# Kernel optimization log

Measured on AMD Instinct MI355X. Metric: run time of the kernel, lower is better.

Reference implementation:

```python
import jax, jax.numpy as jnp
import numpy as np

D_MODEL = 2048
HEADS = 16


def setup_inputs() -> dict:
    key = jax.random.key(0)
    ks = jax.random.split(key, 9)
    s = 1.0 / np.sqrt(D_MODEL)
    x = jax.random.normal(ks[0], (2, 2048, D_MODEL), dtype=jnp.float32)
    wq = jax.random.uniform(ks[1], (D_MODEL, D_MODEL), jnp.float32, -s, s)
    wk = jax.random.uniform(ks[2], (D_MODEL, D_MODEL), jnp.float32, -s, s)
    wv = jax.random.uniform(ks[3], (D_MODEL, D_MODEL), jnp.float32, -s, s)
    wo = jax.random.uniform(ks[4], (D_MODEL, D_MODEL), jnp.float32, -s, s)
    bq = jax.random.uniform(ks[5], (D_MODEL,), jnp.float32, -s, s)
    bk = jax.random.uniform(ks[6], (D_MODEL,), jnp.float32, -s, s)
    bv = jax.random.uniform(ks[7], (D_MODEL,), jnp.float32, -s, s)
    bo = jax.random.uniform(ks[8], (D_MODEL,), jnp.float32, -s, s)
    return {"x": x, "wq": wq, "bq": bq, "wk": wk, "bk": bk,
            "wv": wv, "bv": bv, "wo": wo, "bo": bo}


def _split(t, heads):
    b, s, d = t.shape
    return t.reshape(b, s, heads, d // heads).transpose(0, 2, 1, 3)  # [b,h,s,dh]


def reference(x, wq, bq, wk, bk, wv, bv, wo, bo):
    q = x @ wq.T + bq
    k = x @ wk.T + bk
    v = x @ wv.T + bv
    q, k, v = _split(q, HEADS), _split(k, HEADS), _split(v, HEADS)
    dh = q.shape[-1]
    scale = 1.0 / np.sqrt(dh).astype(np.float32)
    score = jnp.einsum('bhqd,bhkd->bhqk', q, k) * scale  # [b,h,s,s]
    score = jax.nn.softmax(score.astype(jnp.float32), axis=-1).astype(q.dtype)
    out = jnp.einsum('bhqk,bhkd->bhqd', score, v)
    b, h, s, _ = out.shape
    out = out.transpose(0, 2, 1, 3).reshape(b, s, h * dh)
    return out @ wo.T + bo
```

## Files before the change

kernel.cpp:

```cpp
#include <hip/hip_runtime.h>
#include <cstdint>
#include <cstddef>

#define D_MODEL 2048
#define SEQ 2048
#define BATCH 2
#define HEADS 16
#define DH 128
#define MROWS (BATCH * SEQ)

typedef __attribute__((ext_vector_type(8))) short short8;
typedef __attribute__((ext_vector_type(4))) float f32x4;
typedef __attribute__((ext_vector_type(16))) float f32x16;
typedef __attribute__((ext_vector_type(2))) unsigned int uint2e;

__device__ __forceinline__ unsigned short f2bf(float f) {
    unsigned int u = __builtin_bit_cast(unsigned int, f);
    u += 0x7fffu + ((u >> 16) & 1u);
    return (unsigned short)(u >> 16);
}

__device__ __forceinline__ unsigned int cvt_pk_bf16(float lo, float hi) {
    unsigned int w;
    asm("v_cvt_pk_bf16_f32 %0, %1, %2" : "=v"(w) : "v"(lo), "v"(hi));
    return w;
}

__device__ __forceinline__ void swap32(unsigned int& x, unsigned int& y) {
#if __has_builtin(__builtin_amdgcn_permlane32_swap)
    uint2e r = __builtin_amdgcn_permlane32_swap(x, y, false, false);
    x = r[0]; y = r[1];
#else
    const int hi = (threadIdx.x >> 5) & 1;
    const unsigned int gx = (unsigned int)__shfl_xor((int)x, 32);
    const unsigned int gy = (unsigned int)__shfl_xor((int)y, 32);
    const unsigned int nx = hi ? gy : x;
    const unsigned int ny = hi ? y : gx;
    x = nx; y = ny;
#endif
}

__device__ __forceinline__ void gload_lds16(const unsigned short* g, unsigned short* l) {
    __builtin_amdgcn_global_load_lds(
        (const __attribute__((address_space(1))) void*)g,
        (__attribute__((address_space(3))) void*)l, 16, 0, 0);
}

__global__ __launch_bounds__(256) void cvt_kernel(const float* __restrict__ in,
                                                  unsigned short* __restrict__ out, int n4) {
    int i = blockIdx.x * 256 + threadIdx.x;
    if (i < n4) {
        const float4 v = reinterpret_cast<const float4*>(in)[i];
        ushort4 o;
        o.x = f2bf(v.x); o.y = f2bf(v.y); o.z = f2bf(v.z); o.w = f2bf(v.w);
        reinterpret_cast<ushort4*>(out)[i] = o;
    }
}

__global__ __launch_bounds__(256) void cvt4_kernel(const float* __restrict__ w0,
                                                   const float* __restrict__ w1,
                                                   const float* __restrict__ w2,
                                                   const float* __restrict__ w3,
                                                   unsigned short* __restrict__ out) {
    const int per = (D_MODEL * D_MODEL) / 4;
    int i = blockIdx.x * 256 + threadIdx.x;
    const int sel = i / per;
    const int off = i - sel * per;
    const float* s = sel == 0 ? w0 : sel == 1 ? w1 : sel == 2 ? w2 : w3;
    const float4 v = reinterpret_cast<const float4*>(s)[off];
    ushort4 o;
    o.x = f2bf(v.x); o.y = f2bf(v.y); o.z = f2bf(v.z); o.w = f2bf(v.w);
    reinterpret_cast<ushort4*>(out)[i] = o;
}

__global__ __launch_bounds__(512, 2)
void gemm8qk(const unsigned short* __restrict__ A,
             const unsigned short* __restrict__ W0,
             const unsigned short* __restrict__ W1,
             const float* __restrict__ b0f,
             const float* __restrict__ b1f,
             unsigned short* __restrict__ O0,
             unsigned short* __restrict__ O1) {
    constexpr int BK = 64;
    constexpr int K = D_MODEL;
    constexpr int NT_N = 16;
    constexpr int NWG = 16 * NT_N;
    __shared__ unsigned short As[2][16384];
    __shared__ unsigned short Bs[2][16384];

    const int tid  = threadIdx.x;
    const int lane = tid & 63;
    const int wid  = tid >> 6;

    const int wk = (blockIdx.x & 7) * (NWG >> 3) + (blockIdx.x >> 3);
    const int nt = wk % NT_N;
    const int mt = wk / NT_N;
    const int m0 = mt * 256;
    const int nsel = nt >> 3;
    const int nloc = (nt & 7) * 256;

    const unsigned short* Bw = nsel ? W1 : W0;
    const float* bias = nsel ? b1f : b0f;

    const int srow = tid >> 3;
    const int sch  = tid & 7;
    const int ssw  = (sch ^ (srow & 7)) * 8;
    const int sd   = srow * 64 + sch * 8;
    const unsigned short* aS[4];
    const unsigned short* bS[4];
#pragma unroll
    for (int j = 0; j < 4; ++j) {
        aS[j] = A  + (size_t)(m0 + j * 64 + srow) * K + ssw;
        bS[j] = Bw + (size_t)(nloc + j * 64 + srow) * K + ssw;
    }

    const int fr = lane & 15, fg = lane >> 4;
    const int wm = wid >> 2, wn = wid & 3;
    int aoffs[2], boffs[2];
#pragma unroll
    for (int ks = 0; ks < 2; ++ks) {
        const int sw = ((ks * 4 + fg) ^ (fr & 7)) * 8;
        aoffs[ks] = (wm * 128 + fr) * 64 + sw;
        boffs[ks] = (wn * 64 + fr) * 64 + sw;
    }

    f32x4 acc[8][4] = {};

#define STG_F(SET, T)                                                \
    gload_lds16(aS[0] + (T) * BK, &As[SET][0 * 4096 + sd]);          \
    gload_lds16(aS[1] + (T) * BK, &As[SET][1 * 4096 + sd]);          \
    gload_lds16(bS[0] + (T) * BK, &Bs[SET][0 * 4096 + sd]);          \
    gload_lds16(bS[1] + (T) * BK, &Bs[SET][1 * 4096 + sd]);
#define STG_L(SET, T)                                                \
    gload_lds16(aS[2] + (T) * BK, &As[SET][2 * 4096 + sd]);          \
    gload_lds16(aS[3] + (T) * BK, &As[SET][3 * 4096 + sd]);          \
    gload_lds16(bS[2] + (T) * BK, &Bs[SET][2 * 4096 + sd]);          \
    gload_lds16(bS[3] + (T) * BK, &Bs[SET][3 * 4096 + sd]);
#define RD_A(DST, SET, HB)                                           \
    _Pragma("unroll") for (int mi = 0; mi < 4; ++mi)                 \
    _Pragma("unroll") for (int ks = 0; ks < 2; ++ks)                 \
        DST[mi][ks] = *(const short8*)&As[SET][(HB) + mi * 1024 + aoffs[ks]];
#define RD_B(DST, SET, NB)                                           \
    _Pragma("unroll") for (int ni = 0; ni < 2; ++ni)                 \
    _Pragma("unroll") for (int ks = 0; ks < 2; ++ks)                 \
        DST[ni][ks] = *(const short8*)&Bs[SET][((NB) + ni) * 1024 + boffs[ks]];
#define PH_MFMA(AF, BF, MB, NB)                                      \
    __builtin_amdgcn_s_barrier();                                    \
    asm volatile("s_waitcnt lgkmcnt(0)" ::: "memory");               \
    __builtin_amdgcn_sched_barrier(0);                               \
    __builtin_amdgcn_s_setprio(1);                                   \
    _Pragma("unroll") for (int ks = 0; ks < 2; ++ks)                 \
    _Pragma("unroll") for (int mi = 0; mi < 4; ++mi)                 \
    _Pragma("unroll") for (int ni = 0; ni < 2; ++ni)                 \
        acc[(MB) + mi][(NB) + ni] = __builtin_amdgcn_mfma_f32_16x16x32_bf16( \
            AF[mi][ks], BF[ni][ks], acc[(MB) + mi][(NB) + ni], 0, 0, 0);     \
    __builtin_amdgcn_s_setprio(0);                                   \
    __builtin_amdgcn_s_barrier();

    STG_F(0, 0)
    STG_L(0, 0)
    STG_F(1, 1)
    asm volatile("s_waitcnt vmcnt(4)" ::: "memory");
    __builtin_amdgcn_s_barrier();

#pragma unroll 1
    for (int j = 0; j < 16; ++j) {
        const int t0 = 2 * j;
        const bool more = (j < 15);
        short8 aF[4][2], aG[4][2], b01[2][2], b23[2][2];
        RD_A(aF, 0, 0)
        RD_B(b01, 0, 0)
        STG_L(1, t0 + 1)
        PH_MFMA(aF, b01, 0, 0)
        RD_B(b23, 0, 2)
        PH_MFMA(aF, b23, 0, 2)
        RD_A(aG, 0, 4096)
        PH_MFMA(aG, b23, 4, 2)
        if (more) {
            STG_F(0, t0 + 2)
            asm volatile("s_waitcnt vmcnt(4)" ::: "memory");
        } else {
            asm volatile("s_waitcnt vmcnt(0)" ::: "memory");
        }
        PH_MFMA(aG, b01, 4, 0)
        RD_A(aF, 1, 0)
        RD_B(b01, 1, 0)
        if (more) { STG_L(0, t0 + 2) }
        PH_MFMA(aF, b01, 0, 0)
        RD_B(b23, 1, 2)
        PH_MFMA(aF, b23, 0, 2)
        RD_A(aG, 1, 4096)
        PH_MFMA(aG, b23, 4, 2)
        if (more) {
            STG_F(1, t0 + 3)
            asm volatile("s_waitcnt vmcnt(4)" ::: "memory");
        }
        PH_MFMA(aG, b01, 4, 0)
    }
#undef STG_F
#undef STG_L
#undef RD_A
#undef RD_B
#undef PH_MFMA

    unsigned short* Co = nsel ? O1 : O0;
#pragma unroll
    for (int mi = 0; mi < 8; ++mi)
#pragma unroll
        for (int ni = 0; ni < 4; ++ni) {
            const int col = nloc + wn * 64 + ni * 16 + fr;
            const float bv = bias[col];
#pragma unroll
            for (int r = 0; r < 4; ++r) {
                const int row = m0 + wm * 128 + mi * 16 + fg * 4 + r;
                Co[(size_t)row * D_MODEL + col] = f2bf(acc[mi][ni][r] + bv);
            }
        }
}

__global__ __launch_bounds__(512, 2)
void gemmV(const unsigned short* __restrict__ Wv,
           const unsigned short* __restrict__ X,
           const float* __restrict__ bvf,
           unsigned short* __restrict__ VT) {
    constexpr int BK = 64;
    constexpr int K = D_MODEL;
    constexpr int NTILES = K / BK;
    constexpr int NWG = 256;
    __shared__ unsigned short As[3][128 * BK];
    __shared__ unsigned short Bs[3][256 * BK];

    const int tid  = threadIdx.x;
    const int lane = tid & 63;
    const int wid  = tid >> 6;

    const int wk = (blockIdx.x & 7) * (NWG >> 3) + (blockIdx.x >> 3);
    const int nt = wk & 15;
    const int mt = wk >> 4;
    const int m0 = mt * 128;
    const int n0 = nt * 256;

    const int srow = tid >> 3;
    const int sch  = tid & 7;
    const int ssw  = (sch ^ (srow & 7)) * 8;
    const int sd   = srow * 64 + sch * 8;
    const unsigned short* aS[2];
#pragma unroll
    for (int j = 0; j < 2; ++j) aS[j] = Wv + (size_t)(m0 + j * 64 + srow) * K + ssw;
    const unsigned short* bS[4];
#pragma unroll
    for (int j = 0; j < 4; ++j) bS[j] = X + (size_t)(n0 + j * 64 + srow) * K + ssw;

    const int fr = lane & 15, fg = lane >> 4;
    const int wm = wid >> 2, wn = wid & 3;
    int aoff[4][2], boff[4][2];
#pragma unroll
    for (int i = 0; i < 4; ++i)
#pragma unroll
        for (int ks = 0; ks < 2; ++ks) {
            const int sw = ((ks * 4 + fg) ^ (fr & 7)) * 8;
            aoff[i][ks] = (wm * 64 + i * 16 + fr) * BK + sw;
            boff[i][ks] = (wn * 64 + i * 16 + fr) * BK + sw;
        }

    f32x4 acc[4][4] = {};

    unsigned short *pA0 = As[0], *pA1 = As[1], *pA2 = As[2];
    unsigned short *pB0 = Bs[0], *pB1 = Bs[1], *pB2 = Bs[2];

#define STG_AV(P, T) { _Pragma("unroll") for (int j = 0; j < 2; ++j) \
        gload_lds16(aS[j] + (T) * BK, (P) + j * 4096 + sd); }
#define STG_BV(P, T) { _Pragma("unroll") for (int j = 0; j < 4; ++j) \
        gload_lds16(bS[j] + (T) * BK, (P) + j * 4096 + sd); }

    STG_AV(pA0, 0) STG_BV(pB0, 0)
    STG_AV(pA1, 1) STG_BV(pB1, 1)
    asm volatile("s_waitcnt vmcnt(6)" ::: "memory");
    __builtin_amdgcn_s_barrier();

#pragma unroll 1
    for (int t = 0; t < NTILES; ++t) {
        const bool more = (t + 2 < NTILES);
        short8 aF[4][2], bF0[2][2];
#pragma unroll
        for (int mi = 0; mi < 4; ++mi)
#pragma unroll
            for (int ks = 0; ks < 2; ++ks)
                aF[mi][ks] = *(const short8*)&pA0[aoff[mi][ks]];
#pragma unroll
        for (int ni = 0; ni < 2; ++ni)
#pragma unroll
            for (int ks = 0; ks < 2; ++ks)
                bF0[ni][ks] = *(const short8*)&pB0[boff[ni][ks]];
        if (more) { STG_AV(pA2, t + 2) STG_BV(pB2, t + 2) }
        asm volatile("s_waitcnt lgkmcnt(0)" ::: "memory");
        __builtin_amdgcn_sched_barrier(0);
        __builtin_amdgcn_s_setprio(1);
#pragma unroll
        for (int ks = 0; ks < 2; ++ks)
#pragma unroll
            for (int mi = 0; mi < 4; ++mi)
#pragma unroll
                for (int ni = 0; ni < 2; ++ni)
                    acc[mi][ni] = __builtin_amdgcn_mfma_f32_16x16x32_bf16(
                        aF[mi][ks], bF0[ni][ks], acc[mi][ni], 0, 0, 0);
        __builtin_amdgcn_s_setprio(0);
        short8 bG[2][2];
#pragma unroll
        for (int ni = 0; ni < 2; ++ni)
#pragma unroll
            for (int ks = 0; ks < 2; ++ks)
                bG[ni][ks] = *(const short8*)&pB0[boff[2 + ni][ks]];
        asm volatile("s_waitcnt lgkmcnt(0)" ::: "memory");
        __builtin_amdgcn_sched_barrier(0);
        __builtin_amdgcn_s_setprio(1);
#pragma unroll
        for (int ks = 0; ks < 2; ++ks)
#pragma unroll
            for (int mi = 0; mi < 4; ++mi)
#pragma unroll
                for (int ni = 0; ni < 2; ++ni)
                    acc[mi][2 + ni] = __builtin_amdgcn_mfma_f32_16x16x32_bf16(
                        aF[mi][ks], bG[ni][ks], acc[mi][2 + ni], 0, 0, 0);
        __builtin_amdgcn_s_setprio(0);
        if (more) asm volatile("s_waitcnt vmcnt(6)" ::: "memory");
        else      asm volatile("s_waitcnt vmcnt(0)" ::: "memory");
        __builtin_amdgcn_s_barrier();
        unsigned short* tA = pA0; pA0 = pA1; pA1 = pA2; pA2 = tA;
        unsigned short* tB = pB0; pB0 = pB1; pB1 = pB2; pB2 = tB;
    }
#undef STG_AV
#undef STG_BV

#pragma unroll
    for (int mi = 0; mi < 4; ++mi)
#pragma unroll
        for (int r = 0; r < 4; ++r) {
            const int row = m0 + wm * 64 + mi * 16 + fg * 4 + r;
            const float bv = bvf[row];
#pragma unroll
            for (int ni = 0; ni < 4; ++ni) {
                const int col = n0 + wn * 64 + ni * 16 + fr;
                VT[(size_t)row * MROWS + col] = f2bf(acc[mi][ni][r] + bv);
            }
        }
}

__global__ __launch_bounds__(512, 2)
void gemmT1(const unsigned short* __restrict__ A,
            const unsigned short* __restrict__ W0,
            const float* __restrict__ b0f,
            float* __restrict__ OF) {
    constexpr int BM = 256, BN = 128, BK = 64;
    constexpr int K = D_MODEL;
    constexpr int NTILES = K / BK;
    constexpr int NT_N = 16;
    constexpr int NWG = (MROWS / BM) * NT_N;
    __shared__ unsigned short As[3][BM * BK];
    __shared__ unsigned short Bs[3][BN * BK];

    const int tid  = threadIdx.x;
    const int lane = tid & 63;
    const int wid  = tid >> 6;

    const int wk = (blockIdx.x & 7) * (NWG >> 3) + (blockIdx.x >> 3);
    const int nt = wk % NT_N;
    const int mt = wk / NT_N;
    const int m0 = mt * BM;
    const int n0 = nt * BN;

    const int srow = tid >> 3;
    const int sch  = tid & 7;
    const int ssw  = (sch ^ (srow & 7)) * 8;
    const int sd   = srow * 64 + sch * 8;
    const unsigned short* aS[4];
#pragma unroll
    for (int j = 0; j < 4; ++j) aS[j] = A + (size_t)(m0 + j * 64 + srow) * K + ssw;
    const unsigned short* bS[2];
#pragma unroll
    for (int j = 0; j < 2; ++j) bS[j] = W0 + (size_t)(n0 + j * 64 + srow) * K + ssw;

    const int fr = lane & 15, fg = lane >> 4;
    const int wm = wid >> 1, wn = wid & 1;
    int aoff[4][2], boff[4][2];
#pragma unroll
    for (int mi = 0; mi < 4; ++mi)
#pragma unroll
        for (int ks = 0; ks < 2; ++ks) {
            aoff[mi][ks] = (wm * 64 + mi * 16 + fr) * BK + ((ks * 4 + fg) ^ (fr & 7)) * 8;
            boff[mi][ks] = (wn * 64 + mi * 16 + fr) * BK + ((ks * 4 + fg) ^ (fr & 7)) * 8;
        }

    f32x4 acc[4][4] = {};

    unsigned short *pA0 = As[0], *pA1 = As[1], *pA2 = As[2];
    unsigned short *pB0 = Bs[0], *pB1 = Bs[1], *pB2 = Bs[2];

#define STG_A3(P, T) { _Pragma("unroll") for (int j = 0; j < 4; ++j) \
        gload_lds16(aS[j] + (T) * BK, (P) + j * 4096 + sd); }
#define STG_B3(P, T) { _Pragma("unroll") for (int j = 0; j < 2; ++j) \
        gload_lds16(bS[j] + (T) * BK, (P) + j * 4096 + sd); }

    STG_A3(pA0, 0) STG_B3(pB0, 0)
    STG_A3(pA1, 1) STG_B3(pB1, 1)
    asm volatile("s_waitcnt vmcnt(6)" ::: "memory");
    __builtin_amdgcn_s_barrier();

#pragma unroll 1
    for (int t = 0; t < NTILES; ++t) {
        const bool more = (t + 2 < NTILES);
        short8 aF[4][2], bF0[2][2];
#pragma unroll
        for (int mi = 0; mi < 4; ++mi)
#pragma unroll
            for (int ks = 0; ks < 2; ++ks)
                aF[mi][ks] = *(const short8*)&pA0[aoff[mi][ks]];
#pragma unroll
        for (int ni = 0; ni < 2; ++ni)
#pragma unroll
            for (int ks = 0; ks < 2; ++ks)
                bF0[ni][ks] = *(const short8*)&pB0[boff[ni][ks]];
        if (more) { STG_A3(pA2, t + 2) STG_B3(pB2, t + 2) }
        asm volatile("s_waitcnt lgkmcnt(0)" ::: "memory");
        __builtin_amdgcn_sched_barrier(0);
        __builtin_amdgcn_s_setprio(1);
#pragma unroll
        for (int ks = 0; ks < 2; ++ks)
#pragma unroll
            for (int mi = 0; mi < 4; ++mi)
#pragma unroll
                for (int ni = 0; ni < 2; ++ni)
                    acc[mi][ni] = __builtin_amdgcn_mfma_f32_16x16x32_bf16(
                        aF[mi][ks], bF0[ni][ks], acc[mi][ni], 0, 0, 0);
        __builtin_amdgcn_s_setprio(0);
        short8 bG[2][2];
#pragma unroll
        for (int ni = 0; ni < 2; ++ni)
#pragma unroll
            for (int ks = 0; ks < 2; ++ks)
                bG[ni][ks] = *(const short8*)&pB0[boff[2 + ni][ks]];
        asm volatile("s_waitcnt lgkmcnt(0)" ::: "memory");
        __builtin_amdgcn_sched_barrier(0);
        __builtin_amdgcn_s_setprio(1);
#pragma unroll
        for (int ks = 0; ks < 2; ++ks)
#pragma unroll
            for (int mi = 0; mi < 4; ++mi)
#pragma unroll
                for (int ni = 0; ni < 2; ++ni)
                    acc[mi][2 + ni] = __builtin_amdgcn_mfma_f32_16x16x32_bf16(
                        aF[mi][ks], bG[ni][ks], acc[mi][2 + ni], 0, 0, 0);
        __builtin_amdgcn_s_setprio(0);
        if (more) asm volatile("s_waitcnt vmcnt(6)" ::: "memory");
        else      asm volatile("s_waitcnt vmcnt(0)" ::: "memory");
        __builtin_amdgcn_s_barrier();
        unsigned short* tA = pA0; pA0 = pA1; pA1 = pA2; pA2 = tA;
        unsigned short* tB = pB0; pB0 = pB1; pB1 = pB2; pB2 = tB;
    }
#undef STG_A3
#undef STG_B3

#pragma unroll
    for (int mi = 0; mi < 4; ++mi)
#pragma unroll
        for (int ni = 0; ni < 4; ++ni) {
            const int col = n0 + wn * 64 + ni * 16 + fr;
            const float bv = b0f[col];
#pragma unroll
            for (int r = 0; r < 4; ++r) {
                const int row = m0 + wm * 64 + mi * 16 + fg * 4 + r;
                OF[(size_t)row * D_MODEL + col] = acc[mi][ni][r] + bv;
            }
        }
}

__global__ __launch_bounds__(256, 2)
void flash_attn3(const unsigned short* __restrict__ Q, const unsigned short* __restrict__ Kg,
                 const unsigned short* __restrict__ VT, unsigned short* __restrict__ O) {
    constexpr int KVB = 64;
    constexpr int NT = SEQ / KVB;
    __shared__ unsigned short Ks[2 * KVB * DH];
    __shared__ unsigned short Vs[2 * DH * KVB];

    const int tid  = threadIdx.x;
    const int lane = tid & 63;
    const int wid  = tid >> 6;
    const int l31  = lane & 31;
    const int hi   = lane >> 5;

    const int qt = blockIdx.x & 15;
    const int bh = blockIdx.x >> 4;
    const int b = bh >> 4, h = bh & 15;
    const int qrow = qt * 128 + wid * 32 + l31;

    const unsigned short* Qp = Q + ((size_t)b * SEQ + qrow) * D_MODEL + h * DH;
    const unsigned short* Kp = Kg + (size_t)b * SEQ * D_MODEL + h * DH;
    const unsigned short* Vp = VT + (size_t)(h * DH) * MROWS + (size_t)b * SEQ;

    short8 qf[8];
#pragma unroll
    for (int kk = 0; kk < 8; ++kk)
        qf[kk] = *(const short8*)(Qp + kk * 16 + hi * 8);

    f32x16 acc[4] = {};
    float m_run = -1e30f, l_run = 0.f;
    const float Cc = 0.088388347648318447f * 1.4426950408889634f;
    const float THR = 8.0f / Cc;

    int co[8];
#pragma unroll
    for (int kk = 0; kk < 8; ++kk) co[kk] = ((kk * 2 + hi) ^ (l31 & 7)) * 8;

    int kroff[4], vroff[4];
#pragma unroll
    for (int q = 0; q < 4; ++q) {
        const int row_l = wid * 16 + q * 4 + (lane >> 4);
        kroff[q] = row_l * D_MODEL + ((lane & 15) ^ (row_l & 7)) * 8;
        const int d_l = wid * 32 + q * 8 + (lane >> 3);
        vroff[q] = d_l * MROWS + ((lane & 7) ^ (d_l & 7)) * 8;
    }
    unsigned short* KsW = Ks + (wid * 16) * DH;
    unsigned short* VsW = Vs + (wid * 32) * KVB;

#pragma unroll
    for (int q = 0; q < 4; ++q) {
        gload_lds16(Kp + kroff[q], KsW + q * 4 * DH);
        gload_lds16(Vp + vroff[q], VsW + q * 8 * KVB);
    }
    __syncthreads();

    for (int t = 0; t < NT; ++t) {
        const int cur = t & 1;
        if (t + 1 < NT) {
            const unsigned short* Kt = Kp + (size_t)((t + 1) * KVB) * D_MODEL;
            const unsigned short* Vt = Vp + (t + 1) * KVB;
            unsigned short* kd = KsW + (cur ^ 1) * (KVB * DH);
            unsigned short* vd = VsW + (cur ^ 1) * (DH * KVB);
#pragma unroll
            for (int q = 0; q < 4; ++q) {
                gload_lds16(Kt + kroff[q], kd + q * 4 * DH);
                gload_lds16(Vt + vroff[q], vd + q * 8 * KVB);
            }
        }
        const unsigned short* Kc = Ks + cur * (KVB * DH);
        const unsigned short* Vc = Vs + cur * (DH * KVB);

        f32x16 st0 = {}, st1 = {};
        __builtin_amdgcn_s_setprio(1);
#pragma unroll
        for (int kk = 0; kk < 8; ++kk) {
            const short8 kf0 = *(const short8*)&Kc[l31 * DH + co[kk]];
            const short8 kf1 = *(const short8*)&Kc[(32 + l31) * DH + co[kk]];
            st0 = __builtin_amdgcn_mfma_f32_32x32x16_bf16(kf0, qf[kk], st0, 0, 0, 0);
            st1 = __builtin_amdgcn_mfma_f32_32x32x16_bf16(kf1, qf[kk], st1, 0, 0, 0);
        }
        __builtin_amdgcn_s_setprio(0);

        float lm = -1e30f;
#pragma unroll
        for (int r = 0; r < 16; ++r) lm = fmaxf(lm, fmaxf(st0[r], st1[r]));
        {
            unsigned int a = __builtin_bit_cast(unsigned int, lm), bb = a;
            swap32(a, bb);
            lm = fmaxf(lm, __builtin_bit_cast(float, hi ? a : bb));
        }
        if (__any(lm > m_run + THR)) {
            const float mn = fmaxf(m_run, lm);
            const float sf = __builtin_amdgcn_exp2f((m_run - mn) * Cc);
            m_run = mn;
            l_run *= sf;
#pragma unroll
            for (int db = 0; db < 4; ++db)
#pragma unroll
                for (int r = 0; r < 16; ++r) acc[db][r] *= sf;
        }
        const float mc = m_run * Cc;
        float p0[16], p1[16];
        float ps = 0.f;
#pragma unroll
        for (int r = 0; r < 16; ++r) {
            p0[r] = __builtin_amdgcn_exp2f(__builtin_fmaf(st0[r], Cc, -mc));
            p1[r] = __builtin_amdgcn_exp2f(__builtin_fmaf(st1[r], Cc, -mc));
            ps += p0[r] + p1[r];
        }
        {
            unsigned int a = __builtin_bit_cast(unsigned int, ps), bb = a;
            swap32(a, bb);
            ps += __builtin_bit_cast(float, hi ? a : bb);
        }
        l_run += ps;

        unsigned int W0[8], W1[8];
#pragma unroll
        for (int tt = 0; tt < 8; ++tt) {
            W0[tt] = cvt_pk_bf16(p0[2 * tt], p0[2 * tt + 1]);
            W1[tt] = cvt_pk_bf16(p1[2 * tt], p1[2 * tt + 1]);
        }
        swap32(W0[0], W0[2]); swap32(W0[1], W0[3]);
        swap32(W0[4], W0[6]); swap32(W0[5], W0[7]);
        swap32(W1[0], W1[2]); swap32(W1[1], W1[3]);
        swap32(W1[4], W1[6]); swap32(W1[5], W1[7]);
        short8 pf[4];
        {
            uint4 f;
            f.x = W0[0]; f.y = W0[1]; f.z = W0[2]; f.w = W0[3];
            pf[0] = __builtin_bit_cast(short8, f);
            f.x = W0[4]; f.y = W0[5]; f.z = W0[6]; f.w = W0[7];
            pf[1] = __builtin_bit_cast(short8, f);
            f.x = W1[0]; f.y = W1[1]; f.z = W1[2]; f.w = W1[3];
            pf[2] = __builtin_bit_cast(short8, f);
            f.x = W1[4]; f.y = W1[5]; f.z = W1[6]; f.w = W1[7];
            pf[3] = __builtin_bit_cast(short8, f);
        }

        __builtin_amdgcn_s_setprio(1);
#pragma unroll
        for (int db = 0; db < 4; ++db) {
#pragma unroll
            for (int kk16 = 0; kk16 < 4; ++kk16) {
                const short8 vf = *(const short8*)&Vc[(db * 32 + l31) * KVB + co[kk16]];
                acc[db] = __builtin_amdgcn_mfma_f32_32x32x16_bf16(vf, pf[kk16], acc[db], 0, 0, 0);
            }
        }
        __builtin_amdgcn_s_setprio(0);
        __syncthreads();
    }

    const float inv_l = 1.0f / l_run;
    unsigned short* Op = O + ((size_t)b * SEQ + qrow) * D_MODEL + h * DH;
#pragma unroll
    for (int db = 0; db < 4; ++db)
#pragma unroll
        for (int g = 0; g < 4; ++g) {
            ushort4 o4;
            o4.x = f2bf(acc[db][4 * g + 0] * inv_l);
            o4.y = f2bf(acc[db][4 * g + 1] * inv_l);
            o4.z = f2bf(acc[db][4 * g + 2] * inv_l);
            o4.w = f2bf(acc[db][4 * g + 3] * inv_l);
            *(ushort4*)(Op + db * 32 + g * 8 + hi * 4) = o4;
        }
}

extern "C" void kernel_launch(void* const* d_in, const int* in_sizes, int n_in,
                              void* d_out, int out_size, void* d_ws, size_t ws_size,
                              hipStream_t stream) {
    (void)in_sizes; (void)n_in; (void)out_size; (void)ws_size;
    const float* x  = (const float*)d_in[0];
    const float* wq = (const float*)d_in[1];
    const float* bq = (const float*)d_in[2];
    const float* wk = (const float*)d_in[3];
    const float* bk = (const float*)d_in[4];
    const float* wv = (const float*)d_in[5];
    const float* bv = (const float*)d_in[6];
    const float* wo = (const float*)d_in[7];
    const float* bo = (const float*)d_in[8];
    float* out = (float*)d_out;

    unsigned short* ws = (unsigned short*)d_ws;
    const size_t NX = (size_t)MROWS * D_MODEL;
    const size_t NW = (size_t)D_MODEL * D_MODEL;
    unsigned short* xb  = ws;
    unsigned short* wqb = xb + NX;
    unsigned short* wkb = wqb + NW;
    unsigned short* wvb = wkb + NW;
    unsigned short* wob = wvb + NW;
    unsigned short* Qb  = wob + NW;
    unsigned short* Kb  = Qb + NX;
    unsigned short* VTb = Kb + NX;
    unsigned short* Ab  = VTb + NX;

    cvt_kernel<<<(unsigned)(NX / 1024), 256, 0, stream>>>(x, xb, (int)(NX / 4));
    cvt4_kernel<<<(unsigned)(4 * NW / 1024), 256, 0, stream>>>(wq, wk, wv, wo, wqb);

    gemm8qk<<<256, 512, 0, stream>>>(xb, wqb, wkb, bq, bk, Qb, Kb);
    gemmV<<<256, 512, 0, stream>>>(wvb, xb, bv, VTb);

    flash_attn3<<<512, 256, 0, stream>>>(Qb, Kb, VTb, Ab);

    gemmT1<<<256, 512, 0, stream>>>(Ab, wob, bo, out);
}
```

Measured before the change: 250.5 us.

## Software-pipeline flash attention: overlap QK of next tile with softmax-PV of previous

Restructures the attention inner loop so that the QK^T MFMAs for tile t+1 are issued alongside the softmax and PV MFMAs for tile t, using ping-pong score registers and a triple-buffered V tile in shared memory. Explicit vmcnt waits and raw barriers replace __syncthreads. The aim is to hide softmax VALU/exp latency behind matrix work and keep MFMA units busy. In exchange it uses more registers for a second score set and more LDS for the extra V buffer, which may reduce occupancy under the 2-blocks launch bound.

After: 250.2 us. No clear change (-0.1%).

```diff
diff --git a/kernel.cpp b/kernel.cpp
--- a/kernel.cpp
+++ b/kernel.cpp
@@ -475,12 +475,14 @@
 }
 
 __global__ __launch_bounds__(256, 2)
-void flash_attn3(const unsigned short* __restrict__ Q, const unsigned short* __restrict__ Kg,
+void flash_attn4(const unsigned short* __restrict__ Q, const unsigned short* __restrict__ Kg,
                  const unsigned short* __restrict__ VT, unsigned short* __restrict__ O) {
     constexpr int KVB = 64;
     constexpr int NT = SEQ / KVB;
-    __shared__ unsigned short Ks[2 * KVB * DH];
-    __shared__ unsigned short Vs[2 * DH * KVB];
+    constexpr int KSZ = KVB * DH;
+    constexpr int VSZ = DH * KVB;
+    __shared__ unsigned short Ks[2 * KSZ];
+    __shared__ unsigned short Vs[3 * VSZ];
 
     const int tid  = threadIdx.x;
     const int lane = tid & 63;
@@ -503,6 +505,7 @@
         qf[kk] = *(const short8*)(Qp + kk * 16 + hi * 8);
 
     f32x16 acc[4] = {};
+    f32x16 sA0, sA1, sB0, sB1;
     float m_run = -1e30f, l_run = 0.f;
     const float Cc = 0.088388347648318447f * 1.4426950408889634f;
     const float THR = 8.0f / Cc;
@@ -519,112 +522,157 @@
         const int d_l = wid * 32 + q * 8 + (lane >> 3);
         vroff[q] = d_l * MROWS + ((lane & 7) ^ (d_l & 7)) * 8;
     }
-    unsigned short* KsW = Ks + (wid * 16) * DH;
-    unsigned short* VsW = Vs + (wid * 32) * KVB;
-
-#pragma unroll
-    for (int q = 0; q < 4; ++q) {
-        gload_lds16(Kp + kroff[q], KsW + q * 4 * DH);
-        gload_lds16(Vp + vroff[q], VsW + q * 8 * KVB);
-    }
-    __syncthreads();
-
-    for (int t = 0; t < NT; ++t) {
-        const int cur = t & 1;
-        if (t + 1 < NT) {
-            const unsigned short* Kt = Kp + (size_t)((t + 1) * KVB) * D_MODEL;
-            const unsigned short* Vt = Vp + (t + 1) * KVB;
-            unsigned short* kd = KsW + (cur ^ 1) * (KVB * DH);
-            unsigned short* vd = VsW + (cur ^ 1) * (DH * KVB);
-#pragma unroll
-            for (int q = 0; q < 4; ++q) {
-                gload_lds16(Kt + kroff[q], kd + q * 4 * DH);
-                gload_lds16(Vt + vroff[q], vd + q * 8 * KVB);
-            }
-        }
-        const unsigned short* Kc = Ks + cur * (KVB * DH);
-        const unsigned short* Vc = Vs + cur * (DH * KVB);
-
-        f32x16 st0 = {}, st1 = {};
-        __builtin_amdgcn_s_setprio(1);
-#pragma unroll
-        for (int kk = 0; kk < 8; ++kk) {
-            const short8 kf0 = *(const short8*)&Kc[l31 * DH + co[kk]];
-            const short8 kf1 = *(const short8*)&Kc[(32 + l31) * DH + co[kk]];
-            st0 = __builtin_amdgcn_mfma_f32_32x32x16_bf16(kf0, qf[kk], st0, 0, 0, 0);
-            st1 = __builtin_amdgcn_mfma_f32_32x32x16_bf16(kf1, qf[kk], st1, 0, 0, 0);
-        }
-        __builtin_amdgcn_s_setprio(0);
-
-        float lm = -1e30f;
-#pragma unroll
-        for (int r = 0; r < 16; ++r) lm = fmaxf(lm, fmaxf(st0[r], st1[r]));
-        {
-            unsigned int a = __builtin_bit_cast(unsigned int, lm), bb = a;
-            swap32(a, bb);
-            lm = fmaxf(lm, __builtin_bit_cast(float, hi ? a : bb));
-        }
-        if (__any(lm > m_run + THR)) {
-            const float mn = fmaxf(m_run, lm);
-            const float sf = __builtin_amdgcn_exp2f((m_run - mn) * Cc);
-            m_run = mn;
-            l_run *= sf;
-#pragma unroll
-            for (int db = 0; db < 4; ++db)
-#pragma unroll
-                for (int r = 0; r < 16; ++r) acc[db][r] *= sf;
-        }
-        const float mc = m_run * Cc;
-        float p0[16], p1[16];
-        float ps = 0.f;
-#pragma unroll
-        for (int r = 0; r < 16; ++r) {
-            p0[r] = __builtin_amdgcn_exp2f(__builtin_fmaf(st0[r], Cc, -mc));
-            p1[r] = __builtin_amdgcn_exp2f(__builtin_fmaf(st1[r], Cc, -mc));
-            ps += p0[r] + p1[r];
-        }
-        {
-            unsigned int a = __builtin_bit_cast(unsigned int, ps), bb = a;
-            swap32(a, bb);
-            ps += __builtin_bit_cast(float, hi ? a : bb);
-        }
-        l_run += ps;
-
-        unsigned int W0[8], W1[8];
-#pragma unroll
-        for (int tt = 0; tt < 8; ++tt) {
-            W0[tt] = cvt_pk_bf16(p0[2 * tt], p0[2 * tt + 1]);
-            W1[tt] = cvt_pk_bf16(p1[2 * tt], p1[2 * tt + 1]);
-        }
-        swap32(W0[0], W0[2]); swap32(W0[1], W0[3]);
-        swap32(W0[4], W0[6]); swap32(W0[5], W0[7]);
-        swap32(W1[0], W1[2]); swap32(W1[1], W1[3]);
-        swap32(W1[4], W1[6]); swap32(W1[5], W1[7]);
-        short8 pf[4];
-        {
-            uint4 f;
-            f.x = W0[0]; f.y = W0[1]; f.z = W0[2]; f.w = W0[3];
-            pf[0] = __builtin_bit_cast(short8, f);
-            f.x = W0[4]; f.y = W0[5]; f.z = W0[6]; f.w = W0[7];
-            pf[1] = __builtin_bit_cast(short8, f);
-            f.x = W1[0]; f.y = W1[1]; f.z = W1[2]; f.w = W1[3];
-            pf[2] = __builtin_bit_cast(short8, f);
-            f.x = W1[4]; f.y = W1[5]; f.z = W1[6]; f.w = W1[7];
-            pf[3] = __builtin_bit_cast(short8, f);
-        }
-
-        __builtin_amdgcn_s_setprio(1);
-#pragma unroll
-        for (int db = 0; db < 4; ++db) {
-#pragma unroll
-            for (int kk16 = 0; kk16 < 4; ++kk16) {
-                const short8 vf = *(const short8*)&Vc[(db * 32 + l31) * KVB + co[kk16]];
-                acc[db] = __builtin_amdgcn_mfma_f32_32x32x16_bf16(vf, pf[kk16], acc[db], 0, 0, 0);
-            }
-        }
-        __builtin_amdgcn_s_setprio(0);
-        __syncthreads();
-    }
+    const int kdst = (wid * 16) * DH;
+    const int vdst = (wid * 32) * KVB;
+
+    unsigned short* pkr = Ks;
+    unsigned short* pkw = Ks + KSZ;
+    unsigned short* pvm1 = Vs + 2 * VSZ;
+    unsigned short* pv0  = Vs;
+    unsigned short* pvw  = Vs + VSZ;
+
+#pragma unroll
+    for (int q = 0; q < 4; ++q) gload_lds16(Kp + kroff[q], pkr + kdst + q * 4 * DH);
+#pragma unroll
+    for (int q = 0; q < 4; ++q) gload_lds16(Vp + vroff[q], pv0 + vdst + q * 8 * KVB);
+
+#define STAGE_T(T1)                                                             \
+    {                                                                           \
+        const unsigned short* Kt = Kp + (size_t)(T1) * KVB * D_MODEL;           \
+        const unsigned short* Vt = Vp + (T1) * KVB;                             \
+        _Pragma("unroll")                                                       \
+        for (int q = 0; q < 4; ++q) gload_lds16(Kt + kroff[q], pkw + kdst + q * 4 * DH); \
+        _Pragma("unroll")                                                       \
+        for (int q = 0; q < 4; ++q) gload_lds16(Vt + vroff[q], pvw + vdst + q * 8 * KVB); \
+    }
+
+#define QK_T(S0, S1)                                                            \
+    {                                                                           \
+        _Pragma("unroll") for (int r = 0; r < 16; ++r) { S0[r] = 0.f; S1[r] = 0.f; } \
+        __builtin_amdgcn_s_setprio(1);                                          \
+        _Pragma("unroll")                                                       \
+        for (int kk = 0; kk < 8; ++kk) {                                        \
+            const short8 kf0 = *(const short8*)&pkr[l31 * DH + co[kk]];         \
+            const short8 kf1 = *(const short8*)&pkr[(32 + l31) * DH + co[kk]];  \
+            S0 = __builtin_amdgcn_mfma_f32_32x32x16_bf16(kf0, qf[kk], S0, 0, 0, 0); \
+            S1 = __builtin_amdgcn_mfma_f32_32x32x16_bf16(kf1, qf[kk], S1, 0, 0, 0); \
+        }                                                                       \
+        __builtin_amdgcn_s_setprio(0);                                          \
+    }
+
+#define SMPV_T(P0, P1)                                                          \
+    {                                                                           \
+        float lm = -1e30f;                                                      \
+        _Pragma("unroll") for (int r = 0; r < 16; ++r) lm = fmaxf(lm, fmaxf(P0[r], P1[r])); \
+        {                                                                       \
+            unsigned int a_ = __builtin_bit_cast(unsigned int, lm), b_ = a_;    \
+            swap32(a_, b_);                                                     \
+            lm = fmaxf(lm, __builtin_bit_cast(float, hi ? a_ : b_));            \
+        }                                                                       \
+        if (__any(lm > m_run + THR)) {                                          \
+            const float mn = fmaxf(m_run, lm);                                  \
+            const float sf = __builtin_amdgcn_exp2f((m_run - mn) * Cc);         \
+            m_run = mn;                                                         \
+            l_run *= sf;                                                        \
+            _Pragma("unroll") for (int db = 0; db < 4; ++db)                    \
+            _Pragma("unroll") for (int r = 0; r < 16; ++r) acc[db][r] *= sf;    \
+        }                                                                       \
+        const float mc = m_run * Cc;                                            \
+        float ps = 0.f;                                                         \
+        _Pragma("unroll")                                                       \
+        for (int r = 0; r < 16; ++r) {                                          \
+            P0[r] = __builtin_amdgcn_exp2f(__builtin_fmaf(P0[r], Cc, -mc));     \
+            P1[r] = __builtin_amdgcn_exp2f(__builtin_fmaf(P1[r], Cc, -mc));     \
+            ps += P0[r] + P1[r];                                                \
+        }                                                                       \
+        {                                                                       \
+            unsigned int a_ = __builtin_bit_cast(unsigned int, ps), b_ = a_;    \
+            swap32(a_, b_);                                                     \
+            ps += __builtin_bit_cast(float, hi ? a_ : b_);                      \
+        }                                                                       \
+        l_run += ps;                                                            \
+        unsigned int W0[8], W1[8];                                              \
+        _Pragma("unroll")                                                       \
+        for (int tt = 0; tt < 8; ++tt) {                                        \
+            W0[tt] = cvt_pk_bf16(P0[2 * tt], P0[2 * tt + 1]);                   \
+            W1[tt] = cvt_pk_bf16(P1[2 * tt], P1[2 * tt + 1]);                   \
+        }                                                                       \
+        swap32(W0[0], W0[2]); swap32(W0[1], W0[3]);                             \
+        swap32(W0[4], W0[6]); swap32(W0[5], W0[7]);                             \
+        swap32(W1[0], W1[2]); swap32(W1[1], W1[3]);                             \
+        swap32(W1[4], W1[6]); swap32(W1[5], W1[7]);                             \
+        short8 pf[4];                                                           \
+        {                                                                       \
+            uint4 f_;                                                           \
+            f_.x = W0[0]; f_.y = W0[1]; f_.z = W0[2]; f_.w = W0[3];             \
+            pf[0] = __builtin_bit_cast(short8, f_);                             \
+            f_.x = W0[4]; f_.y = W0[5]; f_.z = W0[6]; f_.w = W0[7];             \
+            pf[1] = __builtin_bit_cast(short8, f_);                             \
+            f_.x = W1[0]; f_.y = W1[1]; f_.z = W1[2]; f_.w = W1[3];             \
+            pf[2] = __builtin_bit_cast(short8, f_);                             \
+            f_.x = W1[4]; f_.y = W1[5]; f_.z = W1[6]; f_.w = W1[7];             \
+            pf[3] = __builtin_bit_cast(short8, f_);                             \
+        }                                                                       \
+        __builtin_amdgcn_s_setprio(1);                                          \
+        _Pragma("unroll")                                                       \
+        for (int db = 0; db < 4; ++db) {                                        \
+            _Pragma("unroll")                                                   \
+            for (int kk16 = 0; kk16 < 4; ++kk16) {                              \
+                const short8 vf = *(const short8*)&pvm1[(db * 32 + l31) * KVB + co[kk16]]; \
+                acc[db] = __builtin_amdgcn_mfma_f32_32x32x16_bf16(vf, pf[kk16], acc[db], 0, 0, 0); \
+            }                                                                   \
+        }                                                                       \
+        __builtin_amdgcn_s_setprio(0);                                          \
+    }
+
+#define ROTATE_BUFS                                                             \
+    {                                                                           \
+        unsigned short* tk_ = pkr; pkr = pkw; pkw = tk_;                        \
+        unsigned short* tv_ = pvm1; pvm1 = pv0; pv0 = pvw; pvw = tv_;           \
+    }
+
+    STAGE_T(1)
+    asm volatile("s_waitcnt vmcnt(12)" ::: "memory");
+    __builtin_amdgcn_s_barrier();
+    QK_T(sA0, sA1)
+    __builtin_amdgcn_s_barrier();
+    ROTATE_BUFS
+
+#pragma unroll 1
+    for (int j = 0; j < 15; ++j) {
+        const int t1 = 2 * j + 1;
+        STAGE_T(t1 + 1)
+        asm volatile("s_waitcnt vmcnt(12)" ::: "memory");
+        __builtin_amdgcn_s_barrier();
+        QK_T(sB0, sB1)
+        SMPV_T(sA0, sA1)
+        __builtin_amdgcn_s_barrier();
+        ROTATE_BUFS
+
+        STAGE_T(t1 + 2)
+        asm volatile("s_waitcnt vmcnt(12)" ::: "memory");
+        __builtin_amdgcn_s_barrier();
+        QK_T(sA0, sA1)
+        SMPV_T(sB0, sB1)
+        __builtin_amdgcn_s_barrier();
+        ROTATE_BUFS
+    }
+
+    asm volatile("s_waitcnt vmcnt(4)" ::: "memory");
+    __builtin_amdgcn_s_barrier();
+    QK_T(sB0, sB1)
+    SMPV_T(sA0, sA1)
+    __builtin_amdgcn_s_barrier();
+    ROTATE_BUFS
+
+    asm volatile("s_waitcnt vmcnt(0)" ::: "memory");
+    __builtin_amdgcn_s_barrier();
+    SMPV_T(sB0, sB1)
+
+#undef STAGE_T
+#undef QK_T
+#undef SMPV_T
+#undef ROTATE_BUFS
 
     const float inv_l = 1.0f / l_run;
     unsigned short* Op = O + ((size_t)b * SEQ + qrow) * D_MODEL + h * DH;
@@ -675,7 +723,7 @@
     gemm8qk<<<256, 512, 0, stream>>>(xb, wqb, wkb, bq, bk, Qb, Kb);
     gemmV<<<256, 512, 0, stream>>>(wvb, xb, bv, VTb);
 
-    flash_attn3<<<512, 256, 0, stream>>>(Qb, Kb, VTb, Ab);
+    flash_attn4<<<512, 256, 0, stream>>>(Qb, Kb, VTb, Ab);
 
     gemmT1<<<256, 512, 0, stream>>>(Ab, wob, bo, out);
 }
```

## Switch flash attention to 16x16x32 MFMA with 8 waves per block

Applied to the files above, without the earlier changes.

Rewrites the attention kernel to use 16x16x32 bf16 MFMA tiles instead of 32x32x16. Each block now has 8 waves, each handling 16 query rows instead of 32, so the 128-row query tile and the shared K/V loads are split across more waves. This lowers per-wave register pressure and raises occupancy, and the launch bounds are updated to match. In exchange it adds cross-lane shuffles and a register permutation to rebuild the P operand, and each K/V fragment is reused over fewer query rows, which raises LDS read traffic.

New measurement: 264.3 us. 1.05x slower.

```diff
diff --git a/kernel.cpp b/kernel.cpp
--- a/kernel.cpp
+++ b/kernel.cpp
@@ -11,7 +11,6 @@
 
 typedef __attribute__((ext_vector_type(8))) short short8;
 typedef __attribute__((ext_vector_type(4))) float f32x4;
-typedef __attribute__((ext_vector_type(16))) float f32x16;
 typedef __attribute__((ext_vector_type(2))) unsigned int uint2e;
 
 __device__ __forceinline__ unsigned short f2bf(float f) {
@@ -474,91 +473,101 @@
         }
 }
 
-__global__ __launch_bounds__(256, 2)
-void flash_attn3(const unsigned short* __restrict__ Q, const unsigned short* __restrict__ Kg,
+__global__ __launch_bounds__(512, 4)
+void flash_attn5(const unsigned short* __restrict__ Q, const unsigned short* __restrict__ Kg,
                  const unsigned short* __restrict__ VT, unsigned short* __restrict__ O) {
     constexpr int KVB = 64;
     constexpr int NT = SEQ / KVB;
-    __shared__ unsigned short Ks[2 * KVB * DH];
-    __shared__ unsigned short Vs[2 * DH * KVB];
+    constexpr int KSZ = KVB * DH;
+    constexpr int VSZ = DH * KVB;
+    __shared__ unsigned short Ks[2 * KSZ];
+    __shared__ unsigned short Vs[2 * VSZ];
 
     const int tid  = threadIdx.x;
     const int lane = tid & 63;
     const int wid  = tid >> 6;
-    const int l31  = lane & 31;
+    const int fr   = lane & 15;
+    const int fg   = (lane >> 4) & 3;
     const int hi   = lane >> 5;
+    const bool odd = (fg & 1) != 0;
 
     const int qt = blockIdx.x & 15;
     const int bh = blockIdx.x >> 4;
     const int b = bh >> 4, h = bh & 15;
-    const int qrow = qt * 128 + wid * 32 + l31;
+    const int qrow = qt * 128 + wid * 16 + fr;
 
     const unsigned short* Qp = Q + ((size_t)b * SEQ + qrow) * D_MODEL + h * DH;
     const unsigned short* Kp = Kg + (size_t)b * SEQ * D_MODEL + h * DH;
     const unsigned short* Vp = VT + (size_t)(h * DH) * MROWS + (size_t)b * SEQ;
 
-    short8 qf[8];
-#pragma unroll
-    for (int kk = 0; kk < 8; ++kk)
-        qf[kk] = *(const short8*)(Qp + kk * 16 + hi * 8);
-
-    f32x16 acc[4] = {};
+    short8 qf[4];
+#pragma unroll
+    for (int ks = 0; ks < 4; ++ks)
+        qf[ks] = *(const short8*)(Qp + ks * 32 + fg * 8);
+
+    f32x4 acc[8] = {};
     float m_run = -1e30f, l_run = 0.f;
     const float Cc = 0.088388347648318447f * 1.4426950408889634f;
     const float THR = 8.0f / Cc;
 
-    int co[8];
-#pragma unroll
-    for (int kk = 0; kk < 8; ++kk) co[kk] = ((kk * 2 + hi) ^ (l31 & 7)) * 8;
-
-    int kroff[4], vroff[4];
-#pragma unroll
-    for (int q = 0; q < 4; ++q) {
-        const int row_l = wid * 16 + q * 4 + (lane >> 4);
+    int kco[4], vco[2];
+#pragma unroll
+    for (int ks = 0; ks < 4; ++ks) kco[ks] = ((ks * 4 + fg) ^ (fr & 7)) * 8;
+#pragma unroll
+    for (int kk = 0; kk < 2; ++kk) vco[kk] = ((kk * 4 + fg) ^ (fr & 7)) * 8;
+
+    int kroff[2], vroff[2];
+#pragma unroll
+    for (int q = 0; q < 2; ++q) {
+        const int row_l = wid * 8 + q * 4 + (lane >> 4);
         kroff[q] = row_l * D_MODEL + ((lane & 15) ^ (row_l & 7)) * 8;
-        const int d_l = wid * 32 + q * 8 + (lane >> 3);
+        const int d_l = wid * 16 + q * 8 + (lane >> 3);
         vroff[q] = d_l * MROWS + ((lane & 7) ^ (d_l & 7)) * 8;
     }
-    unsigned short* KsW = Ks + (wid * 16) * DH;
-    unsigned short* VsW = Vs + (wid * 32) * KVB;
-
-#pragma unroll
-    for (int q = 0; q < 4; ++q) {
-        gload_lds16(Kp + kroff[q], KsW + q * 4 * DH);
-        gload_lds16(Vp + vroff[q], VsW + q * 8 * KVB);
+    const int kdst = (wid * 8) * DH;
+    const int vdst = (wid * 16) * KVB;
+
+#pragma unroll
+    for (int q = 0; q < 2; ++q) {
+        gload_lds16(Kp + kroff[q], Ks + kdst + q * 4 * DH);
+        gload_lds16(Vp + vroff[q], Vs + vdst + q * 8 * KVB);
     }
     __syncthreads();
 
+#pragma unroll 1
     for (int t = 0; t < NT; ++t) {
         const int cur = t & 1;
         if (t + 1 < NT) {
-            const unsigned short* Kt = Kp + (size_t)((t + 1) * KVB) * D_MODEL;
+            const unsigned short* Kt = Kp + (size_t)(t + 1) * KVB * D_MODEL;
             const unsigned short* Vt = Vp + (t + 1) * KVB;
-            unsigned short* kd = KsW + (cur ^ 1) * (KVB * DH);
-            unsigned short* vd = VsW + (cur ^ 1) * (DH * KVB);
-#pragma unroll
-            for (int q = 0; q < 4; ++q) {
+            unsigned short* kd = Ks + (cur ^ 1) * KSZ + kdst;
+            unsigned short* vd = Vs + (cur ^ 1) * VSZ + vdst;
+#pragma unroll
+            for (int q = 0; q < 2; ++q) {
                 gload_lds16(Kt + kroff[q], kd + q * 4 * DH);
                 gload_lds16(Vt + vroff[q], vd + q * 8 * KVB);
             }
         }
-        const unsigned short* Kc = Ks + cur * (KVB * DH);
-        const unsigned short* Vc = Vs + cur * (DH * KVB);
-
-        f32x16 st0 = {}, st1 = {};
+        const unsigned short* Kc = Ks + cur * KSZ;
+        const unsigned short* Vc = Vs + cur * VSZ;
+
+        f32x4 st[4] = {};
         __builtin_amdgcn_s_setprio(1);
 #pragma unroll
-        for (int kk = 0; kk < 8; ++kk) {
-            const short8 kf0 = *(const short8*)&Kc[l31 * DH + co[kk]];
-            const short8 kf1 = *(const short8*)&Kc[(32 + l31) * DH + co[kk]];
-            st0 = __builtin_amdgcn_mfma_f32_32x32x16_bf16(kf0, qf[kk], st0, 0, 0, 0);
-            st1 = __builtin_amdgcn_mfma_f32_32x32x16_bf16(kf1, qf[kk], st1, 0, 0, 0);
-        }
+        for (int ks = 0; ks < 4; ++ks)
+#pragma unroll
+            for (int kb = 0; kb < 4; ++kb) {
+                const short8 kf = *(const short8*)&Kc[(kb * 16 + fr) * DH + kco[ks]];
+                st[kb] = __builtin_amdgcn_mfma_f32_16x16x32_bf16(kf, qf[ks], st[kb], 0, 0, 0);
+            }
         __builtin_amdgcn_s_setprio(0);
 
         float lm = -1e30f;
 #pragma unroll
-        for (int r = 0; r < 16; ++r) lm = fmaxf(lm, fmaxf(st0[r], st1[r]));
+        for (int kb = 0; kb < 4; ++kb)
+#pragma unroll
+            for (int r = 0; r < 4; ++r) lm = fmaxf(lm, st[kb][r]);
+        lm = fmaxf(lm, __shfl_xor(lm, 16));
         {
             unsigned int a = __builtin_bit_cast(unsigned int, lm), bb = a;
             swap32(a, bb);
@@ -570,19 +579,20 @@
             m_run = mn;
             l_run *= sf;
 #pragma unroll
-            for (int db = 0; db < 4; ++db)
-#pragma unroll
-                for (int r = 0; r < 16; ++r) acc[db][r] *= sf;
+            for (int db = 0; db < 8; ++db)
+#pragma unroll
+                for (int r = 0; r < 4; ++r) acc[db][r] *= sf;
         }
         const float mc = m_run * Cc;
-        float p0[16], p1[16];
         float ps = 0.f;
 #pragma unroll
-        for (int r = 0; r < 16; ++r) {
-            p0[r] = __builtin_amdgcn_exp2f(__builtin_fmaf(st0[r], Cc, -mc));
-            p1[r] = __builtin_amdgcn_exp2f(__builtin_fmaf(st1[r], Cc, -mc));
-            ps += p0[r] + p1[r];
-        }
+        for (int kb = 0; kb < 4; ++kb)
+#pragma unroll
+            for (int r = 0; r < 4; ++r) {
+                st[kb][r] = __builtin_amdgcn_exp2f(__builtin_fmaf(st[kb][r], Cc, -mc));
+                ps += st[kb][r];
+            }
+        ps += __shfl_xor(ps, 16);
         {
             unsigned int a = __builtin_bit_cast(unsigned int, ps), bb = a;
             swap32(a, bb);
@@ -590,37 +600,40 @@
         }
         l_run += ps;
 
-        unsigned int W0[8], W1[8];
-#pragma unroll
-        for (int tt = 0; tt < 8; ++tt) {
-            W0[tt] = cvt_pk_bf16(p0[2 * tt], p0[2 * tt + 1]);
-            W1[tt] = cvt_pk_bf16(p1[2 * tt], p1[2 * tt + 1]);
-        }
-        swap32(W0[0], W0[2]); swap32(W0[1], W0[3]);
-        swap32(W0[4], W0[6]); swap32(W0[5], W0[7]);
-        swap32(W1[0], W1[2]); swap32(W1[1], W1[3]);
-        swap32(W1[4], W1[6]); swap32(W1[5], W1[7]);
-        short8 pf[4];
-        {
-            uint4 f;
-            f.x = W0[0]; f.y = W0[1]; f.z = W0[2]; f.w = W0[3];
-            pf[0] = __builtin_bit_cast(short8, f);
-            f.x = W0[4]; f.y = W0[5]; f.z = W0[6]; f.w = W0[7];
-            pf[1] = __builtin_bit_cast(short8, f);
-            f.x = W1[0]; f.y = W1[1]; f.z = W1[2]; f.w = W1[3];
-            pf[2] = __builtin_bit_cast(short8, f);
-            f.x = W1[4]; f.y = W1[5]; f.z = W1[6]; f.w = W1[7];
-            pf[3] = __builtin_bit_cast(short8, f);
-        }
+        unsigned int W[8], Wp[8];
+#pragma unroll
+        for (int kb = 0; kb < 4; ++kb) {
+            W[kb * 2]     = cvt_pk_bf16(st[kb][0], st[kb][1]);
+            W[kb * 2 + 1] = cvt_pk_bf16(st[kb][2], st[kb][3]);
+        }
+#pragma unroll
+        for (int i = 0; i < 8; ++i) Wp[i] = (unsigned int)__shfl_xor((int)W[i], 16);
+        unsigned int Ui[8], Ri[8];
+#define XCH(I, DN, UP) { unsigned int a_ = (DN), b_ = (UP); swap32(a_, b_); Ui[I] = a_; Ri[I] = b_; }
+        XCH(0, W[0], W[2])   XCH(1, W[1], W[3])
+        XCH(2, W[4], W[6])   XCH(3, W[5], W[7])
+        XCH(4, Wp[0], Wp[2]) XCH(5, Wp[1], Wp[3])
+        XCH(6, Wp[4], Wp[6]) XCH(7, Wp[5], Wp[7])
+#undef XCH
+        uint4 f0, f1;
+        f0.x = hi ? (odd ? Wp[2] : Ui[0]) : (odd ? Ri[4] : W[0]);
+        f0.y = hi ? (odd ? Wp[3] : Ui[1]) : (odd ? Ri[5] : W[1]);
+        f0.z = hi ? (odd ? W[2]  : Ui[4]) : (odd ? Ri[0] : Wp[0]);
+        f0.w = hi ? (odd ? W[3]  : Ui[5]) : (odd ? Ri[1] : Wp[1]);
+        f1.x = hi ? (odd ? Wp[6] : Ui[2]) : (odd ? Ri[6] : W[4]);
+        f1.y = hi ? (odd ? Wp[7] : Ui[3]) : (odd ? Ri[7] : W[5]);
+        f1.z = hi ? (odd ? W[6]  : Ui[6]) : (odd ? Ri[2] : Wp[4]);
+        f1.w = hi ? (odd ? W[7]  : Ui[7]) : (odd ? Ri[3] : Wp[5]);
+        const short8 pf0 = __builtin_bit_cast(short8, f0);
+        const short8 pf1 = __builtin_bit_cast(short8, f1);
 
         __builtin_amdgcn_s_setprio(1);
 #pragma unroll
-        for (int db = 0; db < 4; ++db) {
-#pragma unroll
-            for (int kk16 = 0; kk16 < 4; ++kk16) {
-                const short8 vf = *(const short8*)&Vc[(db * 32 + l31) * KVB + co[kk16]];
-                acc[db] = __builtin_amdgcn_mfma_f32_32x32x16_bf16(vf, pf[kk16], acc[db], 0, 0, 0);
-            }
+        for (int db = 0; db < 8; ++db) {
+            const short8 vf0 = *(const short8*)&Vc[(db * 16 + fr) * KVB + vco[0]];
+            acc[db] = __builtin_amdgcn_mfma_f32_16x16x32_bf16(vf0, pf0, acc[db], 0, 0, 0);
+            const short8 vf1 = *(const short8*)&Vc[(db * 16 + fr) * KVB + vco[1]];
+            acc[db] = __builtin_amdgcn_mfma_f32_16x16x32_bf16(vf1, pf1, acc[db], 0, 0, 0);
         }
         __builtin_amdgcn_s_setprio(0);
         __syncthreads();
@@ -629,16 +642,14 @@
     const float inv_l = 1.0f / l_run;
     unsigned short* Op = O + ((size_t)b * SEQ + qrow) * D_MODEL + h * DH;
 #pragma unroll
-    for (int db = 0; db < 4; ++db)
-#pragma unroll
-        for (int g = 0; g < 4; ++g) {
-            ushort4 o4;
-            o4.x = f2bf(acc[db][4 * g + 0] * inv_l);
-            o4.y = f2bf(acc[db][4 * g + 1] * inv_l);
-            o4.z = f2bf(acc[db][4 * g + 2] * inv_l);
-            o4.w = f2bf(acc[db][4 * g + 3] * inv_l);
-            *(ushort4*)(Op + db * 32 + g * 8 + hi * 4) = o4;
-        }
+    for (int db = 0; db < 8; ++db) {
+        ushort4 o4;
+        o4.x = f2bf(acc[db][0] * inv_l);
+        o4.y = f2bf(acc[db][1] * inv_l);
+        o4.z = f2bf(acc[db][2] * inv_l);
+        o4.w = f2bf(acc[db][3] * inv_l);
+        *(ushort4*)(Op + db * 16 + fg * 4) = o4;
+    }
 }
 
 extern "C" void kernel_launch(void* const* d_in, const int* in_sizes, int n_in,
@@ -675,7 +686,7 @@
     gemm8qk<<<256, 512, 0, stream>>>(xb, wqb, wkb, bq, bk, Qb, Kb);
     gemmV<<<256, 512, 0, stream>>>(wvb, xb, bv, VTb);
 
-    flash_attn3<<<512, 256, 0, stream>>>(Qb, Kb, VTb, Ab);
+    flash_attn5<<<512, 512, 0, stream>>>(Qb, Kb, VTb, Ab);
 
     gemmT1<<<256, 512, 0, stream>>>(Ab, wob, bo, out);
 }
```
